# Performance work log

Hardware: AMD Instinct MI355X
Metric: run time of the kernel (lower is better)

## Reference

```python
import jax, jax.numpy as jnp
import numpy as np

N_NODES = 10000
N_EDGES = 160000
N_GRAPHS = 64
F = 80        # hidden dim
T = 5         # towers
F_OUT = 16    # per-tower post output (80/5)
N_LAYERS = 4
EPS = 1e-6
BN_EPS = 1e-5
STD_EPS = 1e-5


def setup_inputs() -> dict:
    key = jax.random.key(0)
    ks = jax.random.split(key, 12)
    x = jax.random.uniform(ks[0], (N_NODES, 2), dtype=jnp.float32)
    edge_index = jax.random.randint(ks[1], (2, N_EDGES), 0, N_NODES, dtype=jnp.int64)
    batch = jnp.sort(jax.random.randint(ks[2], (N_NODES,), 0, N_GRAPHS, dtype=jnp.int64))

    def w(k, shape, fan_in):
        return (jax.random.normal(k, shape, jnp.float32) / np.float32(np.sqrt(fan_in)))

    return {
        "x": x, "edge_index": edge_index, "batch": batch,
        "pre_lin_W": w(ks[3], (1, F), 1), "pre_lin_b": jnp.zeros((F,), jnp.float32),
        "pre_W": w(ks[4], (N_LAYERS, T, 2 * F, F), 2 * F), "pre_b": jnp.zeros((N_LAYERS, T, F), jnp.float32),
        "post_W": w(ks[5], (N_LAYERS, T, 13 * F, F_OUT), 13 * F), "post_b": jnp.zeros((N_LAYERS, T, F_OUT), jnp.float32),
        "lin_W": w(ks[6], (N_LAYERS, F, F), F), "lin_b": jnp.zeros((N_LAYERS, F), jnp.float32),
        "bn_gamma": jnp.ones((N_LAYERS, F), jnp.float32), "bn_beta": jnp.zeros((N_LAYERS, F), jnp.float32),
        "mlp_lin_W": w(ks[7], (40, 1), 40), "mlp_lin_b": jnp.zeros((1,), jnp.float32),
        "mlp1_W": w(ks[8], (40, 20), 40), "mlp1_b": jnp.zeros((20,), jnp.float32),
        "mlp2_W": w(ks[9], (20, 1), 20), "mlp2_b": jnp.zeros((1,), jnp.float32),
    }


def _pna_conv(h, src, dst, deg, avg_log_deg, preW, preb, postW, postb, linW, linb):
    # h: [N, F]; messages per tower: pre MLP over cat(x_i, x_j)  (divide_input=False)
    N = h.shape[0]
    hm = jnp.concatenate([h[dst], h[src]], axis=-1)            # [E, 2F]
    m = jnp.einsum('ef,tfo->eto', hm, preW) + preb             # [E, T, F]

    cnt = jnp.maximum(deg, 1.0)[:, None, None]                 # [N,1,1]
    has = (deg > 0)[:, None, None]
    s = jax.ops.segment_sum(m, dst, num_segments=N)
    mean = s / cnt
    mean_sq = jax.ops.segment_sum(m * m, dst, num_segments=N) / cnt
    mn = jax.ops.segment_min(m, dst, num_segments=N)
    mx = jax.ops.segment_max(m, dst, num_segments=N)
    mn = jnp.where(has, mn, 0.0)
    mx = jnp.where(has, mx, 0.0)
    std = jnp.sqrt(jax.nn.relu(mean_sq - mean * mean) + STD_EPS)
    agg = jnp.concatenate([mean, mn, mx, std], axis=-1)        # [N, T, 4F]

    logd = jnp.log(jnp.maximum(deg, 1.0) + 1.0)[:, None, None]
    amp = agg * (logd / avg_log_deg)
    att = agg * (avg_log_deg / logd)
    out = jnp.concatenate([agg, amp, att], axis=-1)            # [N, T, 12F]

    xt = jnp.broadcast_to(h[:, None, :], (N, T, F))
    out = jnp.concatenate([xt, out], axis=-1)                  # [N, T, 13F]
    out = jnp.einsum('ntf,tfo->nto', out, postW) + postb       # [N, T, F_OUT]
    out = out.reshape(N, T * F_OUT)                            # [N, 80]
    return out @ linW + linb


def _forward(x, edge_index, batch, pre_lin_W, pre_lin_b, pre_W, pre_b,
             post_W, post_b, lin_W, lin_b, bn_gamma, bn_beta,
             mlp_lin_W, mlp_lin_b, mlp1_W, mlp1_b, mlp2_W, mlp2_b):
    N = x.shape[0]
    src, dst = edge_index[0], edge_index[1]
    deg = jax.ops.segment_sum(jnp.ones_like(dst, jnp.float32), dst, num_segments=N)
    avg_log_deg = jnp.mean(jnp.log(deg + 1.0))                 # PNA avg log-degree from deg histogram

    operation = x[:, 0:1]
    assignment = x[:, 1:2]
    op = operation @ pre_lin_W + pre_lin_b                     # [N, 80]

    for l in range(N_LAYERS):
        y = _pna_conv(op, src, dst, deg, avg_log_deg,
                      pre_W[l], pre_b[l], post_W[l], post_b[l], lin_W[l], lin_b[l])
        mu = jnp.mean(y, axis=0)
        var = jnp.mean((y - mu) ** 2, axis=0)                  # biased, training-mode BN
        y = (y - mu) / jnp.sqrt(var + BN_EPS) * bn_gamma[l] + bn_beta[l]
        op = jax.nn.relu(y)

    front, behind = op[:, :40], op[:, 40:]
    xc = front * assignment + behind                           # [N, 40], non-negative

    # LastLayer: log-space scatter-add message passing
    log_score = jax.ops.segment_sum(jnp.log(xc[src] + EPS), dst, num_segments=N)
    xc = jnp.exp(log_score + jnp.log(xc + EPS))

    # global mean pool over graphs
    gcnt = jnp.maximum(jax.ops.segment_sum(jnp.ones_like(batch, jnp.float32), batch, num_segments=N_GRAPHS), 1.0)
    pooled = jax.ops.segment_sum(xc, batch, num_segments=N_GRAPHS) / gcnt[:, None]  # [B, 40]

    x_lin = pooled @ mlp_lin_W + mlp_lin_b
    x_cv = pooled @ mlp1_W + mlp1_b
    x_cv = 20.0 - jax.nn.relu(x_cv)
    x_cv = x_cv @ mlp2_W + mlp2_b
    return x_cv + x_lin                                        # [B, 1]


def reference(x, edge_index, batch, pre_lin_W, pre_lin_b, pre_W, pre_b,
              post_W, post_b, lin_W, lin_b, bn_gamma, bn_beta,
              mlp_lin_W, mlp_lin_b, mlp1_W, mlp1_b, mlp2_W, mlp2_b):
    return _forward(x, edge_index, batch, pre_lin_W, pre_lin_b, pre_W, pre_b,
                    post_W, post_b, lin_W, lin_b, bn_gamma, bn_beta,
                    mlp_lin_W, mlp_lin_b, mlp1_W, mlp1_b, mlp2_W, mlp2_b)
```

## Files before the change

kernel.cpp:

```cpp
#include <hip/hip_runtime.h>
#include <math.h>

#define NN 10000
#define NE 160000
#define NG 64
#define FEAT 80
#define NT 5
#define NL 4

__global__ void k_cnt2(const int* __restrict__ dst, const int* __restrict__ batch,
                       int* __restrict__ deg, int* __restrict__ gcnt) {
    int e = blockIdx.x * 256 + threadIdx.x;
    if (e < NE) atomicAdd(&deg[dst[e]], 1);
    if (e < NN) atomicAdd(&gcnt[batch[e]], 1);
}

__global__ void k_scan(const int* __restrict__ deg, int* __restrict__ offs) {
    __shared__ int sums[256];
    int tid = threadIdx.x;
    int start = tid * 40, stop = min(start + 40, NN);
    int s = 0;
    for (int i = start; i < stop; ++i) s += deg[i];
    sums[tid] = s;
    __syncthreads();
    for (int off = 1; off < 256; off <<= 1) {
        int v = (tid >= off) ? sums[tid - off] : 0;
        __syncthreads();
        sums[tid] += v;
        __syncthreads();
    }
    int base = (tid == 0) ? 0 : sums[tid - 1];
    for (int i = start; i < stop; ++i) { offs[i] = base; base += deg[i]; }
    if (tid == 255) offs[NN] = sums[255];
}

__global__ void k_ald(const int* __restrict__ deg, float* __restrict__ ald) {
    __shared__ float red[256];
    int i = blockIdx.x * 256 + threadIdx.x;
    red[threadIdx.x] = (i < NN) ? logf((float)deg[i] + 1.0f) : 0.0f;
    __syncthreads();
    for (int s = 128; s > 0; s >>= 1) {
        if (threadIdx.x < s) red[threadIdx.x] += red[threadIdx.x + s];
        __syncthreads();
    }
    if (threadIdx.x == 0) atomicAdd(ald, red[0]);
}

__global__ void k_fill(const int* __restrict__ src, const int* __restrict__ dst,
                       const int* __restrict__ offs, int* __restrict__ cursor,
                       int* __restrict__ csr) {
    int e = blockIdx.x * 256 + threadIdx.x;
    if (e < NE) {
        int d = dst[e];
        int p = atomicAdd(&cursor[d], 1);
        csr[offs[d] + p] = src[e];
    }
}

__global__ void k_op0(const float* __restrict__ x, const float* __restrict__ plW,
                      const float* __restrict__ plb, float* __restrict__ hT) {
    int i = blockIdx.x * 256 + threadIdx.x;
    if (i < FEAT * NN) {
        int f = i / NN, n = i - f * NN;
        hT[i] = x[2 * n] * plW[f] + plb[f];
    }
}

__global__ __launch_bounds__(256) void k_mm_ab(
        const float* __restrict__ hT, const float* __restrict__ preW_l,
        float* __restrict__ A, float* __restrict__ Bt) {
    __shared__ float hs[16][80];
    int n0 = blockIdx.x * 16;
    int tid = threadIdx.x;
    for (int i = tid; i < 16 * 80; i += 256) {
        int nl = i & 15, f = i >> 4;
        hs[nl][f] = hT[(size_t)f * NN + n0 + nl];
    }
    __syncthreads();
    float acc[4][16];
#pragma unroll
    for (int s = 0; s < 4; s++)
#pragma unroll
        for (int i = 0; i < 16; i++) acc[s][i] = 0.f;
    const float* wp[4];
#pragma unroll
    for (int s = 0; s < 4; s++) {
        int c = tid + s * 256;
        int cs = (c < 800) ? c : 0;
        int part = (cs >= 400) ? 1 : 0;
        int cc = cs - part * 400;
        int t = cc / 80, o = cc - t * 80;
        wp[s] = preW_l + (size_t)(t * 160 + part * 80) * 80 + o;
    }
    for (int fq = 0; fq < 80; fq += 4) {
        float w[4][4];
#pragma unroll
        for (int s = 0; s < 4; s++) {
            w[s][0] = wp[s][(fq + 0) * 80];
            w[s][1] = wp[s][(fq + 1) * 80];
            w[s][2] = wp[s][(fq + 2) * 80];
            w[s][3] = wp[s][(fq + 3) * 80];
        }
#pragma unroll
        for (int i = 0; i < 16; i++) {
            float4 hv = *(const float4*)&hs[i][fq];
#pragma unroll
            for (int s = 0; s < 4; s++) {
                acc[s][i] += hv.x * w[s][0] + hv.y * w[s][1] +
                             hv.z * w[s][2] + hv.w * w[s][3];
            }
        }
    }
#pragma unroll
    for (int s = 0; s < 4; s++) {
        int c = tid + s * 256;
        if (c < 800) {
            int part = (c >= 400) ? 1 : 0;
            int cc = c - part * 400;
            int t = cc / 80, o = cc - t * 80;
            if (part == 0) {
#pragma unroll
                for (int i = 0; i < 16; i++) A[(size_t)(n0 + i) * 400 + cc] = acc[s][i];
            } else {
#pragma unroll
                for (int i = 0; i < 16; i++)
                    Bt[((size_t)t * NN + n0 + i) * 80 + o] = acc[s][i];
            }
        }
    }
}

__global__ __launch_bounds__(256) void k_aggpost(
        const float* __restrict__ A, const float* __restrict__ Bt,
        const int* __restrict__ offs, const int* __restrict__ csr,
        const float* __restrict__ preb_l, const float* __restrict__ hT,
        const float* __restrict__ postW_l, const float* __restrict__ postb_l,
        const float* __restrict__ ald_sum, float* __restrict__ y0T) {
    __shared__ float st[320 * 17];
    int tid = threadIdx.x;
    int id = blockIdx.y * 625 + blockIdx.x;
    int xcd = id & 7;
    int slot = id >> 3;
    int base = (xcd <= 5) ? xcd * 391 : 5 * 391 + (xcd - 5) * 390;
    int r = base + slot;
    int t = r / 625;
    int n0 = (r - t * 625) * 16;
    int ni = tid >> 4;
    int cl = tid & 15;
    int n = n0 + ni;
    int e0 = offs[n], e1 = offs[n + 1];
    const float* Bts = Bt + (size_t)t * NN * 80;
    float s[5], q[5], mn[5], mx[5];
#pragma unroll
    for (int k = 0; k < 5; k++) { s[k] = 0.f; q[k] = 0.f; mn[k] = 3.4e38f; mx[k] = -3.4e38f; }
    int e = e0;
    for (; e + 3 < e1; e += 4) {
        const float* br0 = Bts + (size_t)csr[e] * 80 + cl;
        const float* br1 = Bts + (size_t)csr[e + 1] * 80 + cl;
        const float* br2 = Bts + (size_t)csr[e + 2] * 80 + cl;
        const float* br3 = Bts + (size_t)csr[e + 3] * 80 + cl;
#pragma unroll
        for (int k = 0; k < 5; k++) {
            float b0 = br0[k * 16];
            float b1 = br1[k * 16];
            float b2 = br2[k * 16];
            float b3 = br3[k * 16];
            s[k] += (b0 + b1) + (b2 + b3);
            q[k] += (b0 * b0 + b1 * b1) + (b2 * b2 + b3 * b3);
            mn[k] = fminf(mn[k], fminf(fminf(b0, b1), fminf(b2, b3)));
            mx[k] = fmaxf(mx[k], fmaxf(fmaxf(b0, b1), fmaxf(b2, b3)));
        }
    }
    for (; e < e1; ++e) {
        const float* br = Bts + (size_t)csr[e] * 80 + cl;
#pragma unroll
        for (int k = 0; k < 5; k++) {
            float b = br[k * 16];
            s[k] += b; q[k] += b * b;
            mn[k] = fminf(mn[k], b); mx[k] = fmaxf(mx[k], b);
        }
    }
    int d = e1 - e0;
    float degf = (float)d;
    float cnt = fmaxf(degf, 1.f);
#pragma unroll
    for (int k = 0; k < 5; k++) {
        int c = cl + k * 16;
        float a = A[(size_t)n * 400 + t * 80 + c] + preb_l[t * 80 + c];
        float mean = (degf * a + s[k]) / cnt;
        float msq  = (degf * a * a + 2.f * a * s[k] + q[k]) / cnt;
        float sd = sqrtf(fmaxf(msq - mean * mean, 0.f) + 1e-5f);
        float mnr = (d > 0) ? a + mn[k] : 0.f;
        float mxr = (d > 0) ? a + mx[k] : 0.f;
        st[(0 * 80 + c) * 17 + ni] = mean;
        st[(1 * 80 + c) * 17 + ni] = mnr;
        st[(2 * 80 + c) * 17 + ni] = mxr;
        st[(3 * 80 + c) * 17 + ni] = sd;
    }
    __syncthreads();
    int ni2 = tid & 15;
    int og  = (tid >> 4) & 3;
    int js  = tid >> 6;
    const float* W0 = postW_l + (size_t)t * 1040 * 16;
    float a1[4], a2[4], a3[4];
#pragma unroll
    for (int i = 0; i < 4; i++) { a1[i] = 0.f; a2[i] = 0.f; a3[i] = 0.f; }
    int jb = js * 80;
#pragma unroll 2
    for (int j = jb; j < jb + 80; ++j) {
        float a = st[j * 17 + ni2];
        float4 w1 = *(const float4*)(W0 + (size_t)(80 + j) * 16 + og * 4);
        float4 w2 = *(const float4*)(W0 + (size_t)(400 + j) * 16 + og * 4);
        float4 w3 = *(const float4*)(W0 + (size_t)(720 + j) * 16 + og * 4);
        a1[0] += a * w1.x; a1[1] += a * w1.y; a1[2] += a * w1.z; a1[3] += a * w1.w;
        a2[0] += a * w2.x; a2[1] += a * w2.y; a2[2] += a * w2.z; a2[3] += a * w2.w;
        a3[0] += a * w3.x; a3[1] += a * w3.y; a3[2] += a * w3.z; a3[3] += a * w3.w;
    }
    int fb = js * 20;
#pragma unroll 2
    for (int f = fb; f < fb + 20; ++f) {
        float hv = hT[(size_t)f * NN + n0 + ni2];
        float4 w0 = *(const float4*)(W0 + (size_t)f * 16 + og * 4);
        a1[0] += hv * w0.x; a1[1] += hv * w0.y; a1[2] += hv * w0.z; a1[3] += hv * w0.w;
    }
    __syncthreads();
    float* red = st;
#pragma unroll
    for (int i = 0; i < 4; i++) {
        red[tid * 12 + i]     = a1[i];
        red[tid * 12 + 4 + i] = a2[i];
        red[tid * 12 + 8 + i] = a3[i];
    }
    __syncthreads();
    if (tid < 64) {
        int ni3 = tid & 15, og3 = tid >> 4;
        float b1[4], b2[4], b3[4];
#pragma unroll
        for (int i = 0; i < 4; i++) { b1[i] = 0.f; b2[i] = 0.f; b3[i] = 0.f; }
#pragma unroll
        for (int js3 = 0; js3 < 4; ++js3) {
            const float* rr = red + (size_t)(ni3 + 16 * (og3 + 4 * js3)) * 12;
#pragma unroll
            for (int i = 0; i < 4; i++) {
                b1[i] += rr[i]; b2[i] += rr[4 + i]; b3[i] += rr[8 + i];
            }
        }
        int nw = n0 + ni3;
        float dw = (float)(offs[nw + 1] - offs[nw]);
        float ald = ald_sum[0] * (1.f / NN);
        float logd = logf(fmaxf(dw, 1.f) + 1.f);
        float c1 = logd / ald;
        float c2 = ald / logd;
#pragma unroll
        for (int i = 0; i < 4; i++) {
            int o = og3 * 4 + i;
            float v = b1[i] + c1 * b2[i] + c2 * b3[i] + postb_l[t * 16 + o];
            y0T[(size_t)(t * 16 + o) * NN + nw] = v;
        }
    }
}

__global__ __launch_bounds__(256) void k_lin(
        const float* __restrict__ y0T, const float* __restrict__ linW_l,
        const float* __restrict__ linb_l, float* __restrict__ yT) {
    __shared__ float ws[80 * 8];
    int tid = threadIdx.x;
    int f0 = blockIdx.y * 8;
    for (int idx = tid; idx < 80 * 8; idx += 256)
        ws[idx] = linW_l[(idx >> 3) * 80 + f0 + (idx & 7)];
    __syncthreads();
    int n = blockIdx.x * 256 + tid;
    bool alive = (n < NN);
    int nc = alive ? n : 0;
    float acc[8];
#pragma unroll
    for (int i = 0; i < 8; i++) acc[i] = 0.f;
#pragma unroll 8
    for (int k = 0; k < 80; ++k) {
        float v = y0T[(size_t)k * NN + nc];
        const float4 wa = *(const float4*)(ws + k * 8);
        const float4 wb = *(const float4*)(ws + k * 8 + 4);
        acc[0] += v * wa.x; acc[1] += v * wa.y; acc[2] += v * wa.z; acc[3] += v * wa.w;
        acc[4] += v * wb.x; acc[5] += v * wb.y; acc[6] += v * wb.z; acc[7] += v * wb.w;
    }
    if (alive) {
#pragma unroll
        for (int i = 0; i < 8; i++)
            yT[(size_t)(f0 + i) * NN + n] = acc[i] + linb_l[f0 + i];
    }
}

__global__ void k_bnstats(const float* __restrict__ yT, float* __restrict__ bnst) {
    __shared__ float r1[256], r2[256];
    int f = blockIdx.x;
    int seg = blockIdx.y;
    int tid = threadIdx.x;
    int i0 = seg * 1250, i1 = min(i0 + 1250, NN);
    float s = 0.f, q = 0.f;
    for (int i = i0 + tid; i < i1; i += 256) {
        float v = yT[(size_t)f * NN + i];
        s += v; q += v * v;
    }
    r1[tid] = s; r2[tid] = q;
    __syncthreads();
    for (int st = 128; st > 0; st >>= 1) {
        if (tid < st) { r1[tid] += r1[tid + st]; r2[tid] += r2[tid + st]; }
        __syncthreads();
    }
    if (tid == 0) {
        unsafeAtomicAdd(&bnst[f], r1[0]);
        unsafeAtomicAdd(&bnst[80 + f], r2[0]);
    }
}

__global__ void k_bn(const float* __restrict__ yT, const float* __restrict__ bnst,
                     const float* __restrict__ gamma_l, const float* __restrict__ beta_l,
                     float* __restrict__ hT) {
    int i = blockIdx.x * 256 + threadIdx.x;
    if (i >= FEAT * NN) return;
    int f = i / NN;
    float mu = bnst[f] * (1.f / NN);
    float msq = bnst[80 + f] * (1.f / NN);
    float var = fmaxf(msq - mu * mu, 0.f);
    float v = (yT[i] - mu) * (1.f / sqrtf(var + 1e-5f)) * gamma_l[f] + beta_l[f];
    hT[i] = fmaxf(v, 0.f);
}

__global__ void k_bnxc(const float* __restrict__ yT, const float* __restrict__ bnst,
                       const float* __restrict__ gamma_l, const float* __restrict__ beta_l,
                       const float* __restrict__ x, float* __restrict__ lxc) {
    int i = blockIdx.x * 256 + threadIdx.x;
    if (i >= 40 * NN) return;
    int f = i / NN, n = i - f * NN;
    int f2 = f + 40;
    float mu1 = bnst[f] * (1.f / NN);
    float ms1 = bnst[80 + f] * (1.f / NN);
    float v1 = (yT[(size_t)f * NN + n] - mu1) *
               (1.f / sqrtf(fmaxf(ms1 - mu1 * mu1, 0.f) + 1e-5f)) * gamma_l[f] + beta_l[f];
    v1 = fmaxf(v1, 0.f);
    float mu2 = bnst[f2] * (1.f / NN);
    float ms2 = bnst[80 + f2] * (1.f / NN);
    float v2 = (yT[(size_t)f2 * NN + n] - mu2) *
               (1.f / sqrtf(fmaxf(ms2 - mu2 * mu2, 0.f) + 1e-5f)) * gamma_l[f2] + beta_l[f2];
    v2 = fmaxf(v2, 0.f);
    lxc[(size_t)n * 40 + f] = logf(v1 * x[2 * n + 1] + v2 + 1e-6f);
}

__global__ void k_logagg(const float* __restrict__ lxc, const int* __restrict__ offs,
                         const int* __restrict__ csr, const int* __restrict__ batch,
                         float* __restrict__ pooled) {
    int n = blockIdx.x;
    int tid = threadIdx.x;
    if (tid >= 40) return;
    int e0 = offs[n], e1 = offs[n + 1];
    float s = 0.f;
    for (int k = e0; k < e1; ++k) s += lxc[(size_t)csr[k] * 40 + tid];
    float v = expf(s + lxc[(size_t)n * 40 + tid]);
    atomicAdd(&pooled[batch[n] * 40 + tid], v);
}

__global__ void k_final(const float* __restrict__ pooled, const int* __restrict__ gcnt,
                        const float* __restrict__ mlW, const float* __restrict__ mlb,
                        const float* __restrict__ m1W, const float* __restrict__ m1b,
                        const float* __restrict__ m2W, const float* __restrict__ m2b,
                        float* __restrict__ out) {
    int g = threadIdx.x;
    if (g >= NG) return;
    float inv = 1.f / fmaxf((float)gcnt[g], 1.f);
    float pl[40];
#pragma unroll
    for (int j = 0; j < 40; j++) pl[j] = pooled[g * 40 + j] * inv;
    float xl = mlb[0];
#pragma unroll
    for (int j = 0; j < 40; j++) xl += pl[j] * mlW[j];
    float acc = m2b[0];
    for (int k = 0; k < 20; k++) {
        float v = m1b[k];
#pragma unroll
        for (int j = 0; j < 40; j++) v += pl[j] * m1W[j * 20 + k];
        v = 20.f - fmaxf(v, 0.f);
        acc += v * m2W[k];
    }
    out[g] = acc + xl;
}

extern "C" void kernel_launch(void* const* d_in, const int* in_sizes, int n_in,
                              void* d_out, int out_size, void* d_ws, size_t ws_size,
                              hipStream_t stream) {
    const float* x     = (const float*)d_in[0];
    const int*   ei    = (const int*)d_in[1];
    const int*   batch = (const int*)d_in[2];
    const float* plW   = (const float*)d_in[3];
    const float* plb   = (const float*)d_in[4];
    const float* preW  = (const float*)d_in[5];
    const float* preb  = (const float*)d_in[6];
    const float* postW = (const float*)d_in[7];
    const float* postb = (const float*)d_in[8];
    const float* linW  = (const float*)d_in[9];
    const float* linb  = (const float*)d_in[10];
    const float* bnG   = (const float*)d_in[11];
    const float* bnB   = (const float*)d_in[12];
    const float* mlW   = (const float*)d_in[13];
    const float* mlb   = (const float*)d_in[14];
    const float* m1W   = (const float*)d_in[15];
    const float* m1b   = (const float*)d_in[16];
    const float* m2W   = (const float*)d_in[17];
    const float* m2b   = (const float*)d_in[18];
    float* out = (float*)d_out;
    const int* srcp = ei;
    const int* dstp = ei + NE;

    char* p = (char*)d_ws;
    int*   deg    = (int*)(p + 0);
    int*   cursor = (int*)(p + 40000);
    int*   gcnt   = (int*)(p + 80000);
    float* ald    = (float*)(p + 80256);
    float* pooled = (float*)(p + 80272);
    float* bnst   = (float*)(p + 90512);
    int*   offs   = (int*)(p + 93072);
    int*   csr    = (int*)(p + 133088);
    float* hT     = (float*)(p + 773088);
    float* A      = (float*)(p + 3973088);
    float* Bt     = (float*)(p + 19973088);
    float* y0T = (float*)(p + 35973088);
    float* yT  = (float*)(p + 39173088);
    float* lxc = (float*)(p + 42373088);

    hipMemsetAsync(d_ws, 0, 93072, stream);
    k_cnt2<<<dim3((NE + 255) / 256), 256, 0, stream>>>(dstp, batch, deg, gcnt);
    k_scan<<<1, 256, 0, stream>>>(deg, offs);
    k_ald<<<dim3((NN + 255) / 256), 256, 0, stream>>>(deg, ald);
    k_fill<<<dim3((NE + 255) / 256), 256, 0, stream>>>(srcp, dstp, offs, cursor, csr);
    k_op0<<<dim3((FEAT * NN + 255) / 256), 256, 0, stream>>>(x, plW, plb, hT);

    for (int l = 0; l < NL; ++l) {
        const float* preW_l  = preW  + (size_t)l * NT * 160 * 80;
        const float* preb_l  = preb  + l * NT * 80;
        const float* postW_l = postW + (size_t)l * NT * 1040 * 16;
        const float* postb_l = postb + l * NT * 16;
        const float* linW_l  = linW  + l * 80 * 80;
        const float* linb_l  = linb  + l * 80;
        float* bnst_l = bnst + l * 160;
        k_mm_ab<<<dim3(625), 256, 0, stream>>>(hT, preW_l, A, Bt);
        k_aggpost<<<dim3(625, 5), 256, 0, stream>>>(A, Bt, offs, csr, preb_l,
                                                    hT, postW_l, postb_l, ald, y0T);
        k_lin<<<dim3(40, 10), 256, 0, stream>>>(y0T, linW_l, linb_l, yT);
        k_bnstats<<<dim3(80, 8), 256, 0, stream>>>(yT, bnst_l);
        if (l < NL - 1) {
            k_bn<<<dim3((FEAT * NN + 255) / 256), 256, 0, stream>>>(
                yT, bnst_l, bnG + l * 80, bnB + l * 80, hT);
        } else {
            k_bnxc<<<dim3((40 * NN + 255) / 256), 256, 0, stream>>>(
                yT, bnst_l, bnG + l * 80, bnB + l * 80, x, lxc);
        }
    }

    k_logagg<<<dim3(NN), 64, 0, stream>>>(lxc, offs, csr, batch, pooled);
    k_final<<<1, 64, 0, stream>>>(pooled, gcnt, mlW, mlb, m1W, m1b, m2W, m2b, out);
}
```

Baseline: 876.8 us.

## Register-block post-MLP in aggpost with shared-memory weight tiles

Rewrites the post-tower matmul inside the aggregation kernel. Each thread now accumulates 4 nodes x 4 outputs x 3 scaler parts, and the weights are staged in shared-memory tiles instead of being fetched per thread from global memory. This is meant to cut global weight traffic and raise FMA-to-load intensity. In exchange it adds many block barriers, a 48-float register accumulator, and a 16-way cross-group reduction that only 16 threads perform serially. Output stores become float4-wide.

```diff
diff --git a/kernel.cpp b/kernel.cpp
--- a/kernel.cpp
+++ b/kernel.cpp
@@ -137,6 +137,7 @@
         const float* __restrict__ postW_l, const float* __restrict__ postb_l,
         const float* __restrict__ ald_sum, float* __restrict__ y0T) {
     __shared__ float st[320 * 17];
+    __shared__ float wbuf[32 * 48];
     int tid = threadIdx.x;
     int id = blockIdx.y * 625 + blockIdx.x;
     int xcd = id & 7;
@@ -198,64 +199,103 @@
         st[(3 * 80 + c) * 17 + ni] = sd;
     }
     __syncthreads();
-    int ni2 = tid & 15;
-    int og  = (tid >> 4) & 3;
-    int js  = tid >> 6;
+    int ng = tid & 3;
+    int og = (tid >> 2) & 3;
+    int js = tid >> 4;
     const float* W0 = postW_l + (size_t)t * 1040 * 16;
-    float a1[4], a2[4], a3[4];
-#pragma unroll
-    for (int i = 0; i < 4; i++) { a1[i] = 0.f; a2[i] = 0.f; a3[i] = 0.f; }
-    int jb = js * 80;
-#pragma unroll 2
-    for (int j = jb; j < jb + 80; ++j) {
-        float a = st[j * 17 + ni2];
-        float4 w1 = *(const float4*)(W0 + (size_t)(80 + j) * 16 + og * 4);
-        float4 w2 = *(const float4*)(W0 + (size_t)(400 + j) * 16 + og * 4);
-        float4 w3 = *(const float4*)(W0 + (size_t)(720 + j) * 16 + og * 4);
-        a1[0] += a * w1.x; a1[1] += a * w1.y; a1[2] += a * w1.z; a1[3] += a * w1.w;
-        a2[0] += a * w2.x; a2[1] += a * w2.y; a2[2] += a * w2.z; a2[3] += a * w2.w;
-        a3[0] += a * w3.x; a3[1] += a * w3.y; a3[2] += a * w3.z; a3[3] += a * w3.w;
-    }
-    int fb = js * 20;
-#pragma unroll 2
-    for (int f = fb; f < fb + 20; ++f) {
-        float hv = hT[(size_t)f * NN + n0 + ni2];
-        float4 w0 = *(const float4*)(W0 + (size_t)f * 16 + og * 4);
-        a1[0] += hv * w0.x; a1[1] += hv * w0.y; a1[2] += hv * w0.z; a1[3] += hv * w0.w;
-    }
-    __syncthreads();
+    float af[48];
+#pragma unroll
+    for (int k = 0; k < 48; k++) af[k] = 0.f;
+    for (int tile = 0; tile < 10; ++tile) {
+        for (int idx4 = tid; idx4 < 384; idx4 += 256) {
+            int j_loc = idx4 / 12;
+            int rem = idx4 - j_loc * 12;
+            int p = rem >> 2, o4 = rem & 3;
+            int pofs = (p == 0) ? 80 : (p == 1) ? 400 : 720;
+            int jg = tile * 32 + j_loc;
+            *(float4*)&wbuf[j_loc * 48 + p * 16 + o4 * 4] =
+                *(const float4*)(W0 + (size_t)(pofs + jg) * 16 + o4 * 4);
+        }
+        __syncthreads();
+#pragma unroll
+        for (int jl = 0; jl < 2; ++jl) {
+            int j_loc = js * 2 + jl;
+            int jg = tile * 32 + j_loc;
+            const float* sp = st + jg * 17 + ng * 4;
+            float s0 = sp[0], s1 = sp[1], s2 = sp[2], s3 = sp[3];
+#pragma unroll
+            for (int p = 0; p < 3; ++p) {
+                float4 w = *(const float4*)&wbuf[j_loc * 48 + p * 16 + og * 4];
+                af[p * 16 + 0 * 4 + 0] += s0 * w.x; af[p * 16 + 0 * 4 + 1] += s0 * w.y;
+                af[p * 16 + 0 * 4 + 2] += s0 * w.z; af[p * 16 + 0 * 4 + 3] += s0 * w.w;
+                af[p * 16 + 1 * 4 + 0] += s1 * w.x; af[p * 16 + 1 * 4 + 1] += s1 * w.y;
+                af[p * 16 + 1 * 4 + 2] += s1 * w.z; af[p * 16 + 1 * 4 + 3] += s1 * w.w;
+                af[p * 16 + 2 * 4 + 0] += s2 * w.x; af[p * 16 + 2 * 4 + 1] += s2 * w.y;
+                af[p * 16 + 2 * 4 + 2] += s2 * w.z; af[p * 16 + 2 * 4 + 3] += s2 * w.w;
+                af[p * 16 + 3 * 4 + 0] += s3 * w.x; af[p * 16 + 3 * 4 + 1] += s3 * w.y;
+                af[p * 16 + 3 * 4 + 2] += s3 * w.z; af[p * 16 + 3 * 4 + 3] += s3 * w.w;
+            }
+        }
+        __syncthreads();
+    }
+    for (int ht = 0; ht < 5; ++ht) {
+        if (tid < 64) {
+            int f_loc = tid >> 2, o4 = tid & 3;
+            int fg = ht * 16 + f_loc;
+            *(float4*)&wbuf[f_loc * 16 + o4 * 4] =
+                *(const float4*)(W0 + (size_t)fg * 16 + o4 * 4);
+        }
+        __syncthreads();
+        int fg = ht * 16 + js;
+        float4 hv = *(const float4*)&hT[(size_t)fg * NN + n0 + ng * 4];
+        float4 w = *(const float4*)&wbuf[js * 16 + og * 4];
+        af[0 * 4 + 0] += hv.x * w.x; af[0 * 4 + 1] += hv.x * w.y;
+        af[0 * 4 + 2] += hv.x * w.z; af[0 * 4 + 3] += hv.x * w.w;
+        af[1 * 4 + 0] += hv.y * w.x; af[1 * 4 + 1] += hv.y * w.y;
+        af[1 * 4 + 2] += hv.y * w.z; af[1 * 4 + 3] += hv.y * w.w;
+        af[2 * 4 + 0] += hv.z * w.x; af[2 * 4 + 1] += hv.z * w.y;
+        af[2 * 4 + 2] += hv.z * w.z; af[2 * 4 + 3] += hv.z * w.w;
+        af[3 * 4 + 0] += hv.w * w.x; af[3 * 4 + 1] += hv.w * w.y;
+        af[3 * 4 + 2] += hv.w * w.z; af[3 * 4 + 3] += hv.w * w.w;
+        __syncthreads();
+    }
     float* red = st;
 #pragma unroll
-    for (int i = 0; i < 4; i++) {
-        red[tid * 12 + i]     = a1[i];
-        red[tid * 12 + 4 + i] = a2[i];
-        red[tid * 12 + 8 + i] = a3[i];
-    }
-    __syncthreads();
-    if (tid < 64) {
-        int ni3 = tid & 15, og3 = tid >> 4;
-        float b1[4], b2[4], b3[4];
-#pragma unroll
-        for (int i = 0; i < 4; i++) { b1[i] = 0.f; b2[i] = 0.f; b3[i] = 0.f; }
-#pragma unroll
-        for (int js3 = 0; js3 < 4; ++js3) {
-            const float* rr = red + (size_t)(ni3 + 16 * (og3 + 4 * js3)) * 12;
-#pragma unroll
-            for (int i = 0; i < 4; i++) {
-                b1[i] += rr[i]; b2[i] += rr[4 + i]; b3[i] += rr[8 + i];
+    for (int c = 0; c < 4; ++c) {
+#pragma unroll
+        for (int k = 0; k < 12; ++k) red[tid * 12 + k] = af[c * 12 + k];
+        __syncthreads();
+        if (js == 0) {
+            for (int js2 = 1; js2 < 16; ++js2) {
+                const float* rr = red + (size_t)(ng + (og << 2) + (js2 << 4)) * 12;
+#pragma unroll
+                for (int k = 0; k < 12; ++k) af[c * 12 + k] += rr[k];
             }
         }
-        int nw = n0 + ni3;
-        float dw = (float)(offs[nw + 1] - offs[nw]);
+        __syncthreads();
+    }
+    if (js == 0) {
         float ald = ald_sum[0] * (1.f / NN);
-        float logd = logf(fmaxf(dw, 1.f) + 1.f);
-        float c1 = logd / ald;
-        float c2 = ald / logd;
-#pragma unroll
-        for (int i = 0; i < 4; i++) {
-            int o = og3 * 4 + i;
-            float v = b1[i] + c1 * b2[i] + c2 * b3[i] + postb_l[t * 16 + o];
-            y0T[(size_t)(t * 16 + o) * NN + nw] = v;
+        float v[4][4];
+#pragma unroll
+        for (int i = 0; i < 4; ++i) {
+            int nw = n0 + ng * 4 + i;
+            float dw = (float)(offs[nw + 1] - offs[nw]);
+            float logd = logf(fmaxf(dw, 1.f) + 1.f);
+            float c1 = logd / ald;
+            float c2 = ald / logd;
+#pragma unroll
+            for (int qo = 0; qo < 4; ++qo) {
+                int o = og * 4 + qo;
+                v[i][qo] = af[0 + i * 4 + qo] + c1 * af[16 + i * 4 + qo] +
+                           c2 * af[32 + i * 4 + qo] + postb_l[t * 16 + o];
+            }
+        }
+#pragma unroll
+        for (int qo = 0; qo < 4; ++qo) {
+            int o = og * 4 + qo;
+            float4 pack = make_float4(v[0][qo], v[1][qo], v[2][qo], v[3][qo]);
+            *(float4*)&y0T[(size_t)(t * 16 + o) * NN + n0 + ng * 4] = pack;
         }
     }
 }
```

Measured after the change: 821.9 us. -6.3%, faster.
